# Performance work log

Measured on AMD Instinct MI355X. Metric: run time of the kernel, lower is better.

The kernel has to match this reference:

```python
import jax, jax.numpy as jnp
import numpy as np

B, T, C, L = 512, 512, 96, 64   # batch, time steps, num classes (incl. blank), max label len
BLANK = C - 1                   # keras ctc_batch_cost uses last class as blank
EPS = 1e-7                      # epsilon added before log, as in ctc_batch_cost
NEG = -1e30                     # log-space -inf surrogate


def setup_inputs():
    key = jax.random.key(0)
    k1, k2, k3 = jax.random.split(key, 3)
    # y_pred is a softmax output: positive, rows sum to 1
    u = jax.random.uniform(k1, (B, T, C), dtype=jnp.float32, minval=0.1, maxval=1.0)
    y_pred = u / jnp.sum(u, axis=-1, keepdims=True)
    # labels in [0, BLANK), variable lengths, padded with -1 (as the layer expects)
    labels = jax.random.randint(k2, (B, L), 0, C - 1, dtype=jnp.int32)
    lens = jax.random.randint(k3, (B,), L // 2, L + 1, dtype=jnp.int32)
    y_true = jnp.where(jnp.arange(L)[None, :] < lens[:, None], labels, -1)
    return {"y_true": y_true, "y_pred": y_pred}


def _ctc_loss(y_true, y_pred):
    """Per-example CTC negative log-likelihood (forward DP in log space)."""
    y_true = y_true.astype(jnp.int32)
    lbl_len = jnp.sum((y_true != -1).astype(jnp.int32), axis=-1)          # (B,)
    labels = jnp.where(y_true != -1, y_true, 0)                            # (B,L)

    S = 2 * L + 1
    # extended label: blank, l0, blank, l1, ..., blank
    ext = jnp.full((B, S), BLANK, dtype=jnp.int32).at[:, 1::2].set(labels)  # (B,S)
    ext_m2 = jnp.pad(ext[:, :-2], ((0, 0), (2, 0)), constant_values=BLANK)
    can_skip = (ext != BLANK) & (ext != ext_m2)                             # (B,S)

    lp = jnp.log(y_pred.astype(jnp.float32) + EPS)   # (B,T,C) log-probs
    lp_t = jnp.swapaxes(lp, 0, 1)                    # (T,B,C) for scan over time

    emit0 = jnp.take_along_axis(lp_t[0], ext, axis=1)                       # (B,S)
    alpha0 = (jnp.full((B, S), NEG, dtype=jnp.float32)
              .at[:, 0].set(emit0[:, 0])
              .at[:, 1].set(emit0[:, 1]))

    def step(alpha, lpt):
        a1 = jnp.pad(alpha[:, :-1], ((0, 0), (1, 0)), constant_values=NEG)
        a2 = jnp.pad(alpha[:, :-2], ((0, 0), (2, 0)), constant_values=NEG)
        a2 = jnp.where(can_skip, a2, NEG)
        m = jnp.maximum(alpha, jnp.maximum(a1, a2))
        lse = m + jnp.log(jnp.exp(alpha - m) + jnp.exp(a1 - m) + jnp.exp(a2 - m))
        alpha_new = lse + jnp.take_along_axis(lpt, ext, axis=1)
        return alpha_new, None

    alphaT, _ = jax.lax.scan(step, alpha0, lp_t[1:])

    # total log-prob ends at last blank (s=2*len) or last label (s=2*len-1)
    i_blank = (2 * lbl_len)[:, None]
    i_label = jnp.maximum(2 * lbl_len - 1, 0)[:, None]
    a_b = jnp.take_along_axis(alphaT, i_blank, axis=1)[:, 0]
    a_l = jnp.take_along_axis(alphaT, i_label, axis=1)[:, 0]
    return -jnp.logaddexp(a_b, a_l)                                         # (B,)


def reference(y_true, y_pred):
    # layer adds tf.reduce_mean(ctc_batch_cost(...)) as the model loss
    return jnp.mean(_ctc_loss(y_true, y_pred))
```

## Files before the change

kernel.cpp:

```cpp
#include <hip/hip_runtime.h>


#define B_ 512
#define T_ 512
#define C_ 96
#define L_ 64
#define BLANK_ 95
#define EPSF 1e-7f
#define LN2F 0.69314718055994530942f
#define U_ 32
#define CHF_ (U_ * C_)
#define NCH_ (T_ / U_)

template <int CTRL>
__device__ __forceinline__ float dpp_mov(float x) {
    return __int_as_float(
        __builtin_amdgcn_update_dpp(0, __float_as_int(x), CTRL, 0xF, 0xF, true));
}

__device__ __forceinline__ float wave_max(float m) {
    m = fmaxf(m, dpp_mov<0x111>(m));
    m = fmaxf(m, dpp_mov<0x112>(m));
    m = fmaxf(m, dpp_mov<0x114>(m));
    m = fmaxf(m, dpp_mov<0x118>(m));
    m = fmaxf(m, dpp_mov<0x142>(m));
    m = fmaxf(m, dpp_mov<0x143>(m));
    return __int_as_float(__builtin_amdgcn_readlane(__float_as_int(m), 63));
}

__launch_bounds__(64, 1)
__global__ void ctc_loss_kernel(const int* __restrict__ y_true,
                                const float* __restrict__ y_pred,
                                float* __restrict__ part) {
    __shared__ alignas(16) float smem[2][CHF_];
    const int b = blockIdx.x;
    const int lane = threadIdx.x;

    const int yv = y_true[b * L_ + lane];
    const unsigned long long act = __ballot(yv != -1);
    const int len = __popcll(act);
    const int lab = (yv == -1) ? 0 : yv;
    const int lab_prev = __shfl_up(lab, 1);
    const bool cs = (lane == 0) ? true : (lab != lab_prev);

    const float4* g4 = (const float4*)(y_pred + (size_t)b * (T_ * C_));

    float4 s0, s1, s2, s3, s4, s5, s6, s7, s8, s9, s10, s11;
    float el[U_], eb[U_];
    float a_even, a_odd, a128;
    int accum = 0;

    auto load_chunk = [&](int c) {
        const float4* g = g4 + c * (CHF_ / 4) + lane;
        s0 = g[0 * 64];  s1 = g[1 * 64];  s2 = g[2 * 64];  s3 = g[3 * 64];
        s4 = g[4 * 64];  s5 = g[5 * 64];  s6 = g[6 * 64];  s7 = g[7 * 64];
        s8 = g[8 * 64];  s9 = g[9 * 64];  s10 = g[10 * 64]; s11 = g[11 * 64];
    };
    auto store_chunk = [&](int sl) {
        float4* s = (float4*)&smem[sl][0] + lane;
        s[0 * 64] = s0;  s[1 * 64] = s1;  s[2 * 64] = s2;  s[3 * 64] = s3;
        s[4 * 64] = s4;  s[5 * 64] = s5;  s[6 * 64] = s6;  s[7 * 64] = s7;
        s[8 * 64] = s8;  s[9 * 64] = s9;  s[10 * 64] = s10; s[11 * 64] = s11;
    };
    auto read_emis = [&](int sl) {
        const float* base = &smem[sl][0];
#pragma unroll
        for (int k = 0; k < U_; ++k) {
            el[k] = base[k * C_ + lab] + EPSF;
            eb[k] = base[k * C_ + BLANK_] + EPSF;
        }
    };

    auto step = [&](float plv, float pbv) {
        const float po = dpp_mov<0x138>(a_odd);
        const float pos = cs ? po : 0.0f;
        const float ne = (a_even + po) * pbv;
        const float no = (a_odd + a_even + pos) * plv;
        a128 = (a128 + a_odd) * pbv;
        a_even = ne;
        a_odd = no;
    };

    auto renorm = [&]() {
        const float mv = wave_max(fmaxf(fmaxf(a_even, a_odd), a128));
        const int e = ((__float_as_int(mv) >> 23) & 0xFF) - 126;
        const int k = 96 - e;
        a_even = ldexpf(a_even, k);
        a_odd  = ldexpf(a_odd, k);
        a128   = ldexpf(a128, k);
        accum -= k;
    };

    auto body = [&](int c, bool ld) {
        read_emis(c & 1);
        store_chunk((c + 1) & 1);
        if (ld) load_chunk(c + 2);
#pragma unroll
        for (int k = 0; k < U_; ++k) {
            step(el[k], eb[k]);
            if ((k & 7) == 7) renorm();
        }
    };

    load_chunk(0);
    store_chunk(0);
    load_chunk(1);
    read_emis(0);

    store_chunk(1);
    load_chunk(2);
    a_even = (lane == 0) ? eb[0] : 0.0f;
    a_odd  = (lane == 0) ? el[0] : 0.0f;
    a128 = 0.0f;
#pragma unroll
    for (int k = 1; k < U_; ++k) {
        step(el[k], eb[k]);
        if ((k & 7) == 7) renorm();
    }

    for (int c = 1; c <= 13; ++c) body(c, true);
    body(14, false);

    read_emis(1);
#pragma unroll
    for (int k = 0; k < U_; ++k) {
        step(el[k], eb[k]);
        if ((k & 7) == 7) renorm();
    }

    const float al = __shfl(a_odd, len - 1);
    const float ab = (len < L_) ? __shfl(a_even, len)
                                : __shfl(a128, 63);
    if (lane == 0) part[b] = -LN2F * (log2f(ab + al) + (float)accum);
}

__launch_bounds__(512, 1)
__global__ void ctc_reduce_kernel(const float* __restrict__ part,
                                  float* __restrict__ out) {
    __shared__ float sm[B_];
    const int t = threadIdx.x;
    sm[t] = part[t];
    __syncthreads();
#pragma unroll
    for (int s = B_ / 2; s > 0; s >>= 1) {
        if (t < s) sm[t] += sm[t + s];
        __syncthreads();
    }
    if (t == 0) out[0] = sm[0] * (1.0f / B_);
}

extern "C" void kernel_launch(void* const* d_in, const int* in_sizes, int n_in,
                              void* d_out, int out_size, void* d_ws, size_t ws_size,
                              hipStream_t stream) {
    const int* y_true = (const int*)d_in[0];
    const float* y_pred = (const float*)d_in[1];
    float* part = (float*)d_ws;
    float* out = (float*)d_out;
    ctc_loss_kernel<<<B_, 64, 0, stream>>>(y_true, y_pred, part);
    ctc_reduce_kernel<<<1, B_, 0, stream>>>(part, out);
}
```

Measured before the change: 150.8 us.

## Process two batch elements per wave with interleaved CTC recurrences

```diff
diff --git a/kernel.cpp b/kernel.cpp
--- a/kernel.cpp
+++ b/kernel.cpp
@@ -8,7 +8,7 @@
 #define BLANK_ 95
 #define EPSF 1e-7f
 #define LN2F 0.69314718055994530942f
-#define U_ 32
+#define U_ 16
 #define CHF_ (U_ * C_)
 #define NCH_ (T_ / U_)
 
@@ -32,106 +32,145 @@
 __global__ void ctc_loss_kernel(const int* __restrict__ y_true,
                                 const float* __restrict__ y_pred,
                                 float* __restrict__ part) {
-    __shared__ alignas(16) float smem[2][CHF_];
-    const int b = blockIdx.x;
+    __shared__ alignas(16) float smemA[2][CHF_];
+    __shared__ alignas(16) float smemB[2][CHF_];
+    const int blk = blockIdx.x;
+    const int eA = 2 * blk, eB = 2 * blk + 1;
     const int lane = threadIdx.x;
 
-    const int yv = y_true[b * L_ + lane];
-    const unsigned long long act = __ballot(yv != -1);
-    const int len = __popcll(act);
-    const int lab = (yv == -1) ? 0 : yv;
-    const int lab_prev = __shfl_up(lab, 1);
-    const bool cs = (lane == 0) ? true : (lab != lab_prev);
-
-    const float4* g4 = (const float4*)(y_pred + (size_t)b * (T_ * C_));
-
-    float4 s0, s1, s2, s3, s4, s5, s6, s7, s8, s9, s10, s11;
-    float el[U_], eb[U_];
-    float a_even, a_odd, a128;
-    int accum = 0;
-
-    auto load_chunk = [&](int c) {
-        const float4* g = g4 + c * (CHF_ / 4) + lane;
-        s0 = g[0 * 64];  s1 = g[1 * 64];  s2 = g[2 * 64];  s3 = g[3 * 64];
-        s4 = g[4 * 64];  s5 = g[5 * 64];  s6 = g[6 * 64];  s7 = g[7 * 64];
-        s8 = g[8 * 64];  s9 = g[9 * 64];  s10 = g[10 * 64]; s11 = g[11 * 64];
-    };
-    auto store_chunk = [&](int sl) {
-        float4* s = (float4*)&smem[sl][0] + lane;
-        s[0 * 64] = s0;  s[1 * 64] = s1;  s[2 * 64] = s2;  s[3 * 64] = s3;
-        s[4 * 64] = s4;  s[5 * 64] = s5;  s[6 * 64] = s6;  s[7 * 64] = s7;
-        s[8 * 64] = s8;  s[9 * 64] = s9;  s[10 * 64] = s10; s[11 * 64] = s11;
-    };
-    auto read_emis = [&](int sl) {
-        const float* base = &smem[sl][0];
+    const int yvA = y_true[eA * L_ + lane];
+    const int yvB = y_true[eB * L_ + lane];
+    const int lenA = __popcll(__ballot(yvA != -1));
+    const int lenB = __popcll(__ballot(yvB != -1));
+    const int labA = (yvA == -1) ? 0 : yvA;
+    const int labB = (yvB == -1) ? 0 : yvB;
+    const bool csA = (lane == 0) ? true : (labA != __shfl_up(labA, 1));
+    const bool csB = (lane == 0) ? true : (labB != __shfl_up(labB, 1));
+
+    const float4* gA = (const float4*)(y_pred + (size_t)eA * (T_ * C_));
+    const float4* gB = (const float4*)(y_pred + (size_t)eB * (T_ * C_));
+
+    float4 sA0, sA1, sA2, sA3, sA4, sA5;
+    float4 sB0, sB1, sB2, sB3, sB4, sB5;
+    float elA[U_], ebA[U_], elB[U_], ebB[U_];
+    float aeA, aoA, a1A;  int accA = 0;
+    float aeB, aoB, a1B;  int accB = 0;
+
+    auto loadA = [&](int c) {
+        const float4* g = gA + c * (CHF_ / 4) + lane;
+        sA0 = g[0 * 64]; sA1 = g[1 * 64]; sA2 = g[2 * 64];
+        sA3 = g[3 * 64]; sA4 = g[4 * 64]; sA5 = g[5 * 64];
+    };
+    auto loadB = [&](int c) {
+        const float4* g = gB + c * (CHF_ / 4) + lane;
+        sB0 = g[0 * 64]; sB1 = g[1 * 64]; sB2 = g[2 * 64];
+        sB3 = g[3 * 64]; sB4 = g[4 * 64]; sB5 = g[5 * 64];
+    };
+    auto storeA = [&](int sl) {
+        float4* s = (float4*)&smemA[sl][0] + lane;
+        s[0 * 64] = sA0; s[1 * 64] = sA1; s[2 * 64] = sA2;
+        s[3 * 64] = sA3; s[4 * 64] = sA4; s[5 * 64] = sA5;
+    };
+    auto storeB = [&](int sl) {
+        float4* s = (float4*)&smemB[sl][0] + lane;
+        s[0 * 64] = sB0; s[1 * 64] = sB1; s[2 * 64] = sB2;
+        s[3 * 64] = sB3; s[4 * 64] = sB4; s[5 * 64] = sB5;
+    };
+    auto readA = [&](int sl) {
+        const float* base = &smemA[sl][0];
 #pragma unroll
         for (int k = 0; k < U_; ++k) {
-            el[k] = base[k * C_ + lab] + EPSF;
-            eb[k] = base[k * C_ + BLANK_] + EPSF;
+            elA[k] = base[k * C_ + labA] + EPSF;
+            ebA[k] = base[k * C_ + BLANK_] + EPSF;
         }
     };
-
-    auto step = [&](float plv, float pbv) {
-        const float po = dpp_mov<0x138>(a_odd);
-        const float pos = cs ? po : 0.0f;
-        const float ne = (a_even + po) * pbv;
-        const float no = (a_odd + a_even + pos) * plv;
-        a128 = (a128 + a_odd) * pbv;
-        a_even = ne;
-        a_odd = no;
-    };
-
-    auto renorm = [&]() {
-        const float mv = wave_max(fmaxf(fmaxf(a_even, a_odd), a128));
-        const int e = ((__float_as_int(mv) >> 23) & 0xFF) - 126;
-        const int k = 96 - e;
-        a_even = ldexpf(a_even, k);
-        a_odd  = ldexpf(a_odd, k);
-        a128   = ldexpf(a128, k);
-        accum -= k;
+    auto readB = [&](int sl) {
+        const float* base = &smemB[sl][0];
+#pragma unroll
+        for (int k = 0; k < U_; ++k) {
+            elB[k] = base[k * C_ + labB] + EPSF;
+            ebB[k] = base[k * C_ + BLANK_] + EPSF;
+        }
+    };
+
+    auto stepA = [&](float plv, float pbv) {
+        const float po = dpp_mov<0x138>(aoA);
+        const float pos = csA ? po : 0.0f;
+        const float ne = (aeA + po) * pbv;
+        const float no = (aoA + aeA + pos) * plv;
+        a1A = (a1A + aoA) * pbv;
+        aeA = ne; aoA = no;
+    };
+    auto stepB = [&](float plv, float pbv) {
+        const float po = dpp_mov<0x138>(aoB);
+        const float pos = csB ? po : 0.0f;
+        const float ne = (aeB + po) * pbv;
+        const float no = (aoB + aeB + pos) * plv;
+        a1B = (a1B + aoB) * pbv;
+        aeB = ne; aoB = no;
+    };
+
+    auto renA = [&]() {
+        const float mv = wave_max(fmaxf(fmaxf(aeA, aoA), a1A));
+        const int k = 96 - (((__float_as_int(mv) >> 23) & 0xFF) - 126);
+        aeA = ldexpf(aeA, k); aoA = ldexpf(aoA, k); a1A = ldexpf(a1A, k);
+        accA -= k;
+    };
+    auto renB = [&]() {
+        const float mv = wave_max(fmaxf(fmaxf(aeB, aoB), a1B));
+        const int k = 96 - (((__float_as_int(mv) >> 23) & 0xFF) - 126);
+        aeB = ldexpf(aeB, k); aoB = ldexpf(aoB, k); a1B = ldexpf(a1B, k);
+        accB -= k;
     };
 
     auto body = [&](int c, bool ld) {
-        read_emis(c & 1);
-        store_chunk((c + 1) & 1);
-        if (ld) load_chunk(c + 2);
+        readA(c & 1); readB(c & 1);
+        storeA((c + 1) & 1); storeB((c + 1) & 1);
+        if (ld) { loadA(c + 2); loadB(c + 2); }
 #pragma unroll
         for (int k = 0; k < U_; ++k) {
-            step(el[k], eb[k]);
-            if ((k & 7) == 7) renorm();
+            stepA(elA[k], ebA[k]);
+            stepB(elB[k], ebB[k]);
+            if ((k & 7) == 7) { renA(); renB(); }
         }
     };
 
-    load_chunk(0);
-    store_chunk(0);
-    load_chunk(1);
-    read_emis(0);
-
-    store_chunk(1);
-    load_chunk(2);
-    a_even = (lane == 0) ? eb[0] : 0.0f;
-    a_odd  = (lane == 0) ? el[0] : 0.0f;
-    a128 = 0.0f;
+    loadA(0);  loadB(0);
+    storeA(0); storeB(0);
+    loadA(1);  loadB(1);
+    readA(0);  readB(0);
+    storeA(1); storeB(1);
+    loadA(2);  loadB(2);
+
+    aeA = (lane == 0) ? ebA[0] : 0.0f;  aoA = (lane == 0) ? elA[0] : 0.0f;
+    aeB = (lane == 0) ? ebB[0] : 0.0f;  aoB = (lane == 0) ? elB[0] : 0.0f;
+    a1A = 0.0f; a1B = 0.0f;
 #pragma unroll
     for (int k = 1; k < U_; ++k) {
-        step(el[k], eb[k]);
-        if ((k & 7) == 7) renorm();
-    }
-
-    for (int c = 1; c <= 13; ++c) body(c, true);
-    body(14, false);
-
-    read_emis(1);
+        stepA(elA[k], ebA[k]);
+        stepB(elB[k], ebB[k]);
+        if ((k & 7) == 7) { renA(); renB(); }
+    }
+
+    for (int c = 1; c <= 29; ++c) body(c, true);
+    body(30, false);
+
+    readA(1); readB(1);
 #pragma unroll
     for (int k = 0; k < U_; ++k) {
-        step(el[k], eb[k]);
-        if ((k & 7) == 7) renorm();
-    }
-
-    const float al = __shfl(a_odd, len - 1);
-    const float ab = (len < L_) ? __shfl(a_even, len)
-                                : __shfl(a128, 63);
-    if (lane == 0) part[b] = -LN2F * (log2f(ab + al) + (float)accum);
+        stepA(elA[k], ebA[k]);
+        stepB(elB[k], ebB[k]);
+        if ((k & 7) == 7) { renA(); renB(); }
+    }
+
+    const float alA = __shfl(aoA, lenA - 1);
+    const float abA = (lenA < L_) ? __shfl(aeA, lenA) : __shfl(a1A, 63);
+    const float alB = __shfl(aoB, lenB - 1);
+    const float abB = (lenB < L_) ? __shfl(aeB, lenB) : __shfl(a1B, 63);
+    if (lane == 0) {
+        part[eA] = -LN2F * (log2f(abA + alA) + (float)accA);
+        part[eB] = -LN2F * (log2f(abB + alB) + (float)accB);
+    }
 }
 
 __launch_bounds__(512, 1)
@@ -156,6 +195,6 @@
     const float* y_pred = (const float*)d_in[1];
     float* part = (float*)d_ws;
     float* out = (float*)d_out;
-    ctc_loss_kernel<<<B_, 64, 0, stream>>>(y_true, y_pred, part);
+    ctc_loss_kernel<<<B_ / 2, 64, 0, stream>>>(y_true, y_pred, part);
     ctc_reduce_kernel<<<1, B_, 0, stream>>>(part, out);
 }
```

New measurement: 158.7 us. 1.05x slower.

## Split CTC recursion into concurrent forward and backward halves meeting at midpoint

Applied to the files above, without the earlier changes.

```diff
diff --git a/kernel.cpp b/kernel.cpp
--- a/kernel.cpp
+++ b/kernel.cpp
@@ -7,10 +7,10 @@
 #define L_ 64
 #define BLANK_ 95
 #define EPSF 1e-7f
-#define LN2F 0.69314718055994530942f
+#define LN2D 0.6931471805599453
 #define U_ 32
 #define CHF_ (U_ * C_)
-#define NCH_ (T_ / U_)
+#define NCH_ 8
 
 template <int CTRL>
 __device__ __forceinline__ float dpp_mov(float x) {
@@ -28,13 +28,16 @@
     return __int_as_float(__builtin_amdgcn_readlane(__float_as_int(m), 63));
 }
 
-__launch_bounds__(64, 1)
+__launch_bounds__(128, 1)
 __global__ void ctc_loss_kernel(const int* __restrict__ y_true,
                                 const float* __restrict__ y_pred,
                                 float* __restrict__ part) {
-    __shared__ alignas(16) float smem[2][CHF_];
+    __shared__ alignas(16) float smF[2][CHF_];
+    __shared__ alignas(16) float smB[2][CHF_];
+    __shared__ float xchg[132];
     const int b = blockIdx.x;
-    const int lane = threadIdx.x;
+    const int wid = threadIdx.x >> 6;
+    const int lane = threadIdx.x & 63;
 
     const int yv = y_true[b * L_ + lane];
     const unsigned long long act = __ballot(yv != -1);
@@ -43,95 +46,191 @@
     const int lab_prev = __shfl_up(lab, 1);
     const bool cs = (lane == 0) ? true : (lab != lab_prev);
 
-    const float4* g4 = (const float4*)(y_pred + (size_t)b * (T_ * C_));
-
-    float4 s0, s1, s2, s3, s4, s5, s6, s7, s8, s9, s10, s11;
-    float el[U_], eb[U_];
-    float a_even, a_odd, a128;
-    int accum = 0;
-
-    auto load_chunk = [&](int c) {
-        const float4* g = g4 + c * (CHF_ / 4) + lane;
-        s0 = g[0 * 64];  s1 = g[1 * 64];  s2 = g[2 * 64];  s3 = g[3 * 64];
-        s4 = g[4 * 64];  s5 = g[5 * 64];  s6 = g[6 * 64];  s7 = g[7 * 64];
-        s8 = g[8 * 64];  s9 = g[9 * 64];  s10 = g[10 * 64]; s11 = g[11 * 64];
-    };
-    auto store_chunk = [&](int sl) {
-        float4* s = (float4*)&smem[sl][0] + lane;
-        s[0 * 64] = s0;  s[1 * 64] = s1;  s[2 * 64] = s2;  s[3 * 64] = s3;
-        s[4 * 64] = s4;  s[5 * 64] = s5;  s[6 * 64] = s6;  s[7 * 64] = s7;
-        s[8 * 64] = s8;  s[9 * 64] = s9;  s[10 * 64] = s10; s[11 * 64] = s11;
-    };
-    auto read_emis = [&](int sl) {
-        const float* base = &smem[sl][0];
-#pragma unroll
-        for (int k = 0; k < U_; ++k) {
-            el[k] = base[k * C_ + lab] + EPSF;
-            eb[k] = base[k * C_ + BLANK_] + EPSF;
-        }
-    };
-
-    auto step = [&](float plv, float pbv) {
-        const float po = dpp_mov<0x138>(a_odd);
-        const float pos = cs ? po : 0.0f;
-        const float ne = (a_even + po) * pbv;
-        const float no = (a_odd + a_even + pos) * plv;
-        a128 = (a128 + a_odd) * pbv;
-        a_even = ne;
-        a_odd = no;
-    };
-
-    auto renorm = [&]() {
-        const float mv = wave_max(fmaxf(fmaxf(a_even, a_odd), a128));
-        const int e = ((__float_as_int(mv) >> 23) & 0xFF) - 126;
-        const int k = 96 - e;
-        a_even = ldexpf(a_even, k);
-        a_odd  = ldexpf(a_odd, k);
-        a128   = ldexpf(a128, k);
-        accum -= k;
-    };
-
-    auto body = [&](int c, bool ld) {
-        read_emis(c & 1);
-        store_chunk((c + 1) & 1);
-        if (ld) load_chunk(c + 2);
+    float r_ae = 0.0f, r_ao = 0.0f, r_a1 = 0.0f;
+    int r_acc = 0;
+
+    if (wid == 0) {
+        const float4* g4 = (const float4*)(y_pred + (size_t)b * (T_ * C_));
+        float4 s0, s1, s2, s3, s4, s5, s6, s7, s8, s9, s10, s11;
+        float el[U_], eb[U_];
+        float ae, ao, a1;
+        int acc = 0;
+
+        auto load_chunk = [&](int c) {
+            const float4* g = g4 + c * (CHF_ / 4) + lane;
+            s0 = g[0 * 64];  s1 = g[1 * 64];  s2 = g[2 * 64];  s3 = g[3 * 64];
+            s4 = g[4 * 64];  s5 = g[5 * 64];  s6 = g[6 * 64];  s7 = g[7 * 64];
+            s8 = g[8 * 64];  s9 = g[9 * 64];  s10 = g[10 * 64]; s11 = g[11 * 64];
+        };
+        auto store_chunk = [&](int sl) {
+            float4* s = (float4*)&smF[sl][0] + lane;
+            s[0 * 64] = s0;  s[1 * 64] = s1;  s[2 * 64] = s2;  s[3 * 64] = s3;
+            s[4 * 64] = s4;  s[5 * 64] = s5;  s[6 * 64] = s6;  s[7 * 64] = s7;
+            s[8 * 64] = s8;  s[9 * 64] = s9;  s[10 * 64] = s10; s[11 * 64] = s11;
+        };
+        auto read_emis = [&](int sl) {
+            const float* base = &smF[sl][0];
+#pragma unroll
+            for (int k = 0; k < U_; ++k) {
+                el[k] = base[k * C_ + lab] + EPSF;
+                eb[k] = base[k * C_ + BLANK_] + EPSF;
+            }
+        };
+        auto step = [&](float plv, float pbv) {
+            const float po = dpp_mov<0x138>(ao);
+            const float pos = cs ? po : 0.0f;
+            const float ne = (ae + po) * pbv;
+            const float no = (ao + ae + pos) * plv;
+            a1 = (a1 + ao) * pbv;
+            ae = ne;
+            ao = no;
+        };
+        auto renorm = [&]() {
+            const float mv = wave_max(fmaxf(fmaxf(ae, ao), a1));
+            const int k = 96 - (((__float_as_int(mv) >> 23) & 0xFF) - 126);
+            ae = ldexpf(ae, k); ao = ldexpf(ao, k); a1 = ldexpf(a1, k);
+            acc -= k;
+        };
+        auto body = [&](int c, bool ld) {
+            read_emis(c & 1);
+            store_chunk((c + 1) & 1);
+            if (ld) load_chunk(c + 2);
+#pragma unroll
+            for (int k = 0; k < U_; ++k) {
+                step(el[k], eb[k]);
+                if ((k & 7) == 7) renorm();
+            }
+        };
+
+        load_chunk(0);
+        store_chunk(0);
+        load_chunk(1);
+        read_emis(0);
+        store_chunk(1);
+        load_chunk(2);
+        ae = (lane == 0) ? eb[0] : 0.0f;
+        ao = (lane == 0) ? el[0] : 0.0f;
+        a1 = 0.0f;
+#pragma unroll
+        for (int k = 1; k < U_; ++k) {
+            step(el[k], eb[k]);
+            if ((k & 7) == 7) renorm();
+        }
+        for (int c = 1; c <= 5; ++c) body(c, true);
+        body(6, false);
+        read_emis(1);
 #pragma unroll
         for (int k = 0; k < U_; ++k) {
             step(el[k], eb[k]);
             if ((k & 7) == 7) renorm();
         }
-    };
-
-    load_chunk(0);
-    store_chunk(0);
-    load_chunk(1);
-    read_emis(0);
-
-    store_chunk(1);
-    load_chunk(2);
-    a_even = (lane == 0) ? eb[0] : 0.0f;
-    a_odd  = (lane == 0) ? el[0] : 0.0f;
-    a128 = 0.0f;
-#pragma unroll
-    for (int k = 1; k < U_; ++k) {
-        step(el[k], eb[k]);
-        if ((k & 7) == 7) renorm();
+        r_ae = ldexpf(ae, -96); r_ao = ldexpf(ao, -96); r_a1 = ldexpf(a1, -96);
+        r_acc = acc + 96;
+    } else {
+        const float4* g4 = (const float4*)(y_pred + (size_t)b * (T_ * C_));
+        const int labn = __shfl_down(lab, 1);
+        const int csn_i = __shfl_down((int)cs, 1);
+        const float csn_f = csn_i ? 1.0f : 0.0f;
+        const bool is63 = (lane == 63);
+        float4 s0, s1, s2, s3, s4, s5, s6, s7, s8, s9, s10, s11;
+        float el[U_], eb[U_], eq[U_];
+        float be, bo, b1;
+        int acc = -96;
+
+        auto load_chunk = [&](int cc) {
+            const float4* g = g4 + (480 - 32 * cc) * (C_ / 4) + lane;
+            s0 = g[0 * 64];  s1 = g[1 * 64];  s2 = g[2 * 64];  s3 = g[3 * 64];
+            s4 = g[4 * 64];  s5 = g[5 * 64];  s6 = g[6 * 64];  s7 = g[7 * 64];
+            s8 = g[8 * 64];  s9 = g[9 * 64];  s10 = g[10 * 64]; s11 = g[11 * 64];
+        };
+        auto store_chunk = [&](int sl) {
+            float4* s = (float4*)&smB[sl][0] + lane;
+            s[0 * 64] = s0;  s[1 * 64] = s1;  s[2 * 64] = s2;  s[3 * 64] = s3;
+            s[4 * 64] = s4;  s[5 * 64] = s5;  s[6 * 64] = s6;  s[7 * 64] = s7;
+            s[8 * 64] = s8;  s[9 * 64] = s9;  s[10 * 64] = s10; s[11 * 64] = s11;
+        };
+        auto read_emis = [&](int sl) {
+            const float* base = &smB[sl][0];
+#pragma unroll
+            for (int k = 0; k < U_; ++k) {
+                const int rr = (U_ - 1 - k) * C_;
+                el[k] = base[rr + lab] + EPSF;
+                eb[k] = base[rr + BLANK_] + EPSF;
+                eq[k] = csn_f * (base[rr + labn] + EPSF);
+            }
+        };
+        auto step = [&](float el_, float eb_, float eq_) {
+            const float bon = dpp_mov<0x130>(bo);
+            const float ber = dpp_mov<0x130>(be);
+            const float ben = is63 ? b1 : ber;
+            const float t = el_ * bo;
+            const float nbe = eb_ * be + t;
+            const float nbo = t + eb_ * ben + eq_ * bon;
+            b1 = eb_ * b1;
+            be = nbe;
+            bo = nbo;
+        };
+        auto renorm = [&]() {
+            const float mv = wave_max(fmaxf(fmaxf(be, bo), b1));
+            const int k = 96 - (((__float_as_int(mv) >> 23) & 0xFF) - 126);
+            be = ldexpf(be, k); bo = ldexpf(bo, k); b1 = ldexpf(b1, k);
+            acc -= k;
+        };
+        auto body = [&](int c, bool ld) {
+            read_emis(c & 1);
+            store_chunk((c + 1) & 1);
+            if (ld) load_chunk(c + 2);
+#pragma unroll
+            for (int k = 0; k < U_; ++k) {
+                step(el[k], eb[k], eq[k]);
+                if ((k & 7) == 7) renorm();
+            }
+        };
+
+        load_chunk(0);
+        store_chunk(0);
+        load_chunk(1);
+        read_emis(0);
+        store_chunk(1);
+        load_chunk(2);
+        const float K96 = 0x1.0p96f;
+        bo = (lane == len - 1) ? K96 : 0.0f;
+        be = (len < L_ && lane == len) ? K96 : 0.0f;
+        b1 = (len == L_ && is63) ? K96 : 0.0f;
+#pragma unroll
+        for (int k = 0; k < U_; ++k) {
+            step(el[k], eb[k], eq[k]);
+            if ((k & 7) == 7) renorm();
+        }
+        for (int c = 1; c <= 5; ++c) body(c, true);
+        body(6, false);
+        read_emis(1);
+#pragma unroll
+        for (int k = 0; k < U_; ++k) {
+            step(el[k], eb[k], eq[k]);
+            if ((k & 7) == 7) renorm();
+        }
+        xchg[2 * lane] = ldexpf(be, -96);
+        xchg[2 * lane + 1] = ldexpf(bo, -96);
+        if (is63) {
+            xchg[128] = ldexpf(b1, -96);
+            xchg[129] = (float)(acc + 96);
+        }
     }
 
-    for (int c = 1; c <= 13; ++c) body(c, true);
-    body(14, false);
-
-    read_emis(1);
-#pragma unroll
-    for (int k = 0; k < U_; ++k) {
-        step(el[k], eb[k]);
-        if ((k & 7) == 7) renorm();
+    __syncthreads();
+
+    if (wid == 0) {
+        double s = (double)r_ae * (double)xchg[2 * lane]
+                 + (double)r_ao * (double)xchg[2 * lane + 1];
+        if (lane == 63) s += (double)r_a1 * (double)xchg[128];
+#pragma unroll
+        for (int off = 32; off >= 1; off >>= 1) s += __shfl_xor(s, off);
+        if (lane == 0) {
+            const double accB = (double)xchg[129];
+            part[b] = (float)(-LN2D * (log2(s) + (double)r_acc + accB));
+        }
     }
-
-    const float al = __shfl(a_odd, len - 1);
-    const float ab = (len < L_) ? __shfl(a_even, len)
-                                : __shfl(a128, 63);
-    if (lane == 0) part[b] = -LN2F * (log2f(ab + al) + (float)accum);
 }
 
 __launch_bounds__(512, 1)
@@ -156,6 +255,6 @@
     const float* y_pred = (const float*)d_in[1];
     float* part = (float*)d_ws;
     float* out = (float*)d_out;
-    ctc_loss_kernel<<<B_, 64, 0, stream>>>(y_true, y_pred, part);
+    ctc_loss_kernel<<<B_, 128, 0, stream>>>(y_true, y_pred, part);
     ctc_reduce_kernel<<<1, B_, 0, stream>>>(part, out);
 }
```

New measurement: 152.5 us. About the same (+1.1%).
